# Kernel tuning notes

Hardware: AMD Instinct MI355X
Metric: run time of the kernel (lower is better)

## Reference

```python
import jax, jax.numpy as jnp
import numpy as np

H = W = 64          # input_resolution
C = 256             # dim
HEADS = 8
WS = 8              # window_size
SHIFT = WS // 2
DEPTH = 2           # block 0: no shift, block 1: shifted + mask
HIDDEN = 4 * C      # mlp_ratio * dim
B = 8
N = WS * WS                 # tokens per window
NW = (H // WS) * (W // WS)  # windows per image
EPS = 1e-5


def _rel_pos_index():
    coords = np.stack(np.meshgrid(np.arange(WS), np.arange(WS), indexing='ij')).reshape(2, -1)
    rel = (coords[:, :, None] - coords[:, None, :]).transpose(1, 2, 0)
    rel[:, :, 0] += WS - 1
    rel[:, :, 1] += WS - 1
    rel[:, :, 0] *= 2 * WS - 1
    return rel.sum(-1)  # [N, N] indices into (2*ws-1)^2 table

REL_IDX = jnp.asarray(_rel_pos_index())


def _attn_mask():
    # Swin shift mask: label 3x3 regions, compare window-token labels
    img = np.zeros((H, W))
    slices = (slice(0, -WS), slice(-WS, -SHIFT), slice(-SHIFT, None))
    cnt = 0
    for hs in slices:
        for ws_ in slices:
            img[hs, ws_] = cnt
            cnt += 1
    mw = img.reshape(H // WS, WS, W // WS, WS).transpose(0, 2, 1, 3).reshape(-1, N)
    diff = mw[:, None, :] - mw[:, :, None]
    return jnp.asarray(np.where(diff != 0, -100.0, 0.0), dtype=np.float32)  # [nW, N, N]

ATTN_MASK = _attn_mask()


def layernorm(x, g, b):
    mu = jnp.mean(x, axis=-1, keepdims=True)
    var = jnp.mean((x - mu) ** 2, axis=-1, keepdims=True)
    return (x - mu) * jax.lax.rsqrt(var + EPS) * g + b


def setup_inputs() -> dict:
    key = jax.random.key(0)
    ks = jax.random.split(key, 6)
    s = 0.02
    return {
        'x': jax.random.normal(ks[0], (B, H * W, C), jnp.float32),
        'qkv_w': jax.random.normal(ks[1], (DEPTH, C, 3 * C), jnp.float32) * s,
        'qkv_b': jnp.zeros((DEPTH, 3 * C), jnp.float32),
        'proj_w': jax.random.normal(ks[2], (DEPTH, C, C), jnp.float32) * s,
        'proj_b': jnp.zeros((DEPTH, C), jnp.float32),
        'ln1_g': jnp.ones((DEPTH, C), jnp.float32),
        'ln1_b': jnp.zeros((DEPTH, C), jnp.float32),
        'ln2_g': jnp.ones((DEPTH, C), jnp.float32),
        'ln2_b': jnp.zeros((DEPTH, C), jnp.float32),
        'fc1_w': jax.random.normal(ks[3], (DEPTH, C, HIDDEN), jnp.float32) * s,
        'fc1_b': jnp.zeros((DEPTH, HIDDEN), jnp.float32),
        'fc2_w': jax.random.normal(ks[4], (DEPTH, HIDDEN, C), jnp.float32) * s,
        'fc2_b': jnp.zeros((DEPTH, C), jnp.float32),
        'rpb': jax.random.normal(ks[5], (DEPTH, (2 * WS - 1) ** 2, HEADS), jnp.float32) * s,
    }


def window_attention(xw, qw, qb, pw, pb, rpb_i, mask):
    # xw: [B*nW, N, C]
    B_ = xw.shape[0]
    d = C // HEADS
    qkv = (xw @ qw + qb).reshape(B_, N, 3, HEADS, d).transpose(2, 0, 3, 1, 4)
    q, k, v = qkv[0] * (d ** -0.5), qkv[1], qkv[2]   # [B_, h, N, d]
    attn = jnp.einsum('bhnd,bhmd->bhnm', q, k)
    bias = rpb_i[REL_IDX.reshape(-1)].reshape(N, N, HEADS).transpose(2, 0, 1)
    attn = attn + bias[None]
    if mask is not None:
        attn = attn.reshape(-1, NW, HEADS, N, N) + mask[None, :, None]
        attn = attn.reshape(-1, HEADS, N, N)
    attn = jax.nn.softmax(attn, axis=-1)
    out = jnp.einsum('bhnm,bhmd->bhnd', attn, v).transpose(0, 2, 1, 3).reshape(B_, N, C)
    return out @ pw + pb


def reference(x, qkv_w, qkv_b, proj_w, proj_b, ln1_g, ln1_b, ln2_g, ln2_b,
              fc1_w, fc1_b, fc2_w, fc2_b, rpb):
    for i in range(DEPTH):
        shift = 0 if i % 2 == 0 else SHIFT
        mask = None if shift == 0 else ATTN_MASK
        shortcut = x
        h = layernorm(x, ln1_g[i], ln1_b[i]).reshape(-1, H, W, C)
        if shift:
            h = jnp.roll(h, (-shift, -shift), axis=(1, 2))
        # window partition -> [B*nW, N, C]
        hw = h.reshape(-1, H // WS, WS, W // WS, WS, C).transpose(0, 1, 3, 2, 4, 5).reshape(-1, N, C)
        aw = window_attention(hw, qkv_w[i], qkv_b[i], proj_w[i], proj_b[i], rpb[i], mask)
        # window reverse
        h = aw.reshape(-1, H // WS, W // WS, WS, WS, C).transpose(0, 1, 3, 2, 4, 5).reshape(-1, H, W, C)
        if shift:
            h = jnp.roll(h, (shift, shift), axis=(1, 2))
        x = shortcut + h.reshape(-1, H * W, C)
        m = layernorm(x, ln2_g[i], ln2_b[i])
        m = jax.nn.gelu(m @ fc1_w[i] + fc1_b[i], approximate=False) @ fc2_w[i] + fc2_b[i]
        x = x + m
    return x
```

## Files before the change

### kernel.cpp

```cpp
#include <hip/hip_runtime.h>
#include <hip/hip_bf16.h>


typedef __hip_bfloat16 bf16;
typedef unsigned short u16;
typedef unsigned int u32;
typedef short short8 __attribute__((ext_vector_type(8)));
typedef float floatx4 __attribute__((ext_vector_type(4)));

#define DEVI static __device__ __forceinline__
#define WAITCNT_VM(n) asm volatile("s_waitcnt vmcnt(" #n ")" ::: "memory")

DEVI float lo16(u32 u) { union { u32 i; float f; } x; x.i = u << 16; return x.f; }
DEVI float hi16(u32 u) { union { u32 i; float f; } x; x.i = u & 0xffff0000u; return x.f; }
DEVI float b2f(u16 u) { union { u32 i; float f; } x; x.i = ((u32)u) << 16; return x.f; }
DEVI u16 f2b(float f) {
  union { float f; u32 i; } x; x.f = f;
  u32 r = x.i + 0x7fffu + ((x.i >> 16) & 1u);
  return (u16)(r >> 16);
}
DEVI float in_elem(const void* p, size_t i, int m) {
  return m ? b2f(((const u16*)p)[i]) : ((const float*)p)[i];
}
DEVI int swlab(int g) { return (g < 56) ? 0 : (g < 60 ? 1 : 2); }

DEVI float gelu_cheap(float v) {
  const float u = v * v;
  const float t = v * __builtin_fmaf(0.1029436f, u, 2.3022090f);
  const float e = __builtin_amdgcn_exp2f(t);
  const float r = __builtin_amdgcn_rcpf(e + 1.0f);
  return __builtin_fmaf(-v, r, v);
}

DEVI void async16(const bf16* g, bf16* l) {
  __builtin_amdgcn_global_load_lds((const __attribute__((address_space(1))) u32*)g,
                                   (__attribute__((address_space(3))) u32*)l, 16, 0, 0);
}

__global__ void k_detect(const u32* __restrict__ ln1g, int* __restrict__ mode) {
  if (threadIdx.x == 0 && blockIdx.x == 0)
    *mode = (ln1g[0] == 0x3F803F80u) ? 1 : 0;
}

__global__ __launch_bounds__(256) void k_ingest_ln(const void* __restrict__ xin,
    float* __restrict__ xf, const void* __restrict__ gamw, const void* __restrict__ betw,
    bf16* __restrict__ outp, const int* __restrict__ mode)
{
  const int m = *mode;
  const int l = threadIdx.x & 63, w = threadIdx.x >> 6;
  const int row = blockIdx.x * 4 + w;
  const int t = row & 63, win = row >> 6;
  const int bb = win >> 6, wi = win & 63;
  const int gh = ((wi >> 3) << 3) + (t >> 3);
  const int gw = ((wi & 7) << 3) + (t & 7);
  const int srow = (bb << 12) + (gh << 6) + gw;
  const int cb = l << 2;
  float4 v;
  if (m) {
    const uint2 u = *(const uint2*)((const u16*)xin + (size_t)srow * 256 + cb);
    v = make_float4(lo16(u.x), hi16(u.x), lo16(u.y), hi16(u.y));
  } else {
    v = ((const float4*)((const float*)xin + (size_t)srow * 256))[l];
  }
  ((float4*)(xf + (size_t)srow * 256))[l] = v;
  float s = v.x + v.y + v.z + v.w;
#pragma unroll
  for (int off = 32; off > 0; off >>= 1) s += __shfl_xor(s, off, 64);
  const float mu = s * 0.00390625f;
  const float a = v.x - mu, b = v.y - mu, c = v.z - mu, d = v.w - mu;
  float q = a * a + b * b + c * c + d * d;
#pragma unroll
  for (int off = 32; off > 0; off >>= 1) q += __shfl_xor(q, off, 64);
  const float rs = rsqrtf(q * 0.00390625f + 1e-5f);
  const float o0 = a * rs * in_elem(gamw, cb + 0, m) + in_elem(betw, cb + 0, m);
  const float o1 = b * rs * in_elem(gamw, cb + 1, m) + in_elem(betw, cb + 1, m);
  const float o2 = c * rs * in_elem(gamw, cb + 2, m) + in_elem(betw, cb + 2, m);
  const float o3 = d * rs * in_elem(gamw, cb + 3, m) + in_elem(betw, cb + 3, m);
  const u32 p0 = (u32)f2b(o0) | ((u32)f2b(o1) << 16);
  const u32 p1 = (u32)f2b(o2) | ((u32)f2b(o3) << 16);
  *(uint2*)((u16*)outp + (size_t)row * 256 + cb) = make_uint2(p0, p1);
}

__global__ __launch_bounds__(256) void k_transpose(
    const void* __restrict__ src, bf16* __restrict__ dst,
    const int* __restrict__ mode, int estride, int dstride, int R, int Cn) {
  __shared__ float T[32][33];
  const int m = *mode;
  const int tx = threadIdx.x & 31, ty = threadIdx.x >> 5;
  const int bc = blockIdx.x << 5, br = blockIdx.y << 5;
  for (int d = 0; d < 2; ++d) {
    __syncthreads();
#pragma unroll
    for (int dy = 0; dy < 4; ++dy) {
      const int r = br + ty + dy * 8;
      T[ty + dy * 8][tx] = in_elem(src, (size_t)d * estride + (size_t)r * Cn + bc + tx, m);
    }
    __syncthreads();
#pragma unroll
    for (int dy = 0; dy < 4; ++dy) {
      const int c = bc + ty + dy * 8;
      ((u16*)dst)[(size_t)d * dstride + (size_t)c * R + br + tx] = f2b(T[tx][ty + dy * 8]);
    }
  }
}

template <int EPI>
__global__ __launch_bounds__(256, 3) void k_gemm(
    const bf16* __restrict__ A, const bf16* __restrict__ Bt,
    const void* __restrict__ bias, bf16* __restrict__ outb,
    const int* __restrict__ mode, int boff, int K, int N)
{
  __shared__ __align__(16) bf16 As[3][128 * 32];
  __shared__ __align__(16) bf16 Bs[3][128 * 32];
  __shared__ __align__(16) float EPs[4][4][72];
  const int md = *mode;
  const int tid = threadIdx.x;
  const int l = tid & 63, wid = tid >> 6;
  const int wr = wid >> 1, wc = wid & 1;

  const int gx = gridDim.x;
  const int nwg = gx * gridDim.y;
  int fid = blockIdx.y * gx + blockIdx.x;
  if (!(nwg & 7)) fid = (fid & 7) * (nwg >> 3) + (fid >> 3);
  const int row0 = (fid / gx) * 128;
  const int col0 = (fid % gx) * 128;

  const int lrow = l >> 2;
  const int lkof = (((l & 3) ^ ((l >> 3) & 3)) * 8);
  const int qsw  = (((l >> 4) ^ ((l >> 1) & 3)) * 8);

  floatx4 acc[4][4];
#pragma unroll
  for (int mi = 0; mi < 4; ++mi)
#pragma unroll
    for (int ni = 0; ni < 4; ++ni)
      acc[mi][ni] = (floatx4){0.f, 0.f, 0.f, 0.f};

  auto stage = [&](int b, int kbase) {
    const int kk = kbase + lkof;
#pragma unroll
    for (int c = 0; c < 2; ++c) {
      const int seg = c * 4 + wid;
      async16(A + (size_t)(row0 + seg * 16 + lrow) * K + kk, &As[b][seg * 512]);
      async16(Bt + (size_t)(col0 + seg * 16 + lrow) * K + kk, &Bs[b][seg * 512]);
    }
  };

  const int nsl = K >> 5;
  stage(0, 0);
  stage(1, 32);

  for (int s = 0; s < nsl; ++s) {
    const int cur = s % 3;
    if (s < nsl - 1) { WAITCNT_VM(4); }
    else            { WAITCNT_VM(0); }
    __builtin_amdgcn_s_barrier();
    if (s + 2 < nsl) stage((s + 2) % 3, (s + 2) * 32);

    short8 af[4], bq[4];
#pragma unroll
    for (int mi = 0; mi < 4; ++mi)
      af[mi] = *(const short8*)&As[cur][(wr * 64 + mi * 16 + (l & 15)) * 32 + qsw];
#pragma unroll
    for (int ni = 0; ni < 4; ++ni)
      bq[ni] = *(const short8*)&Bs[cur][(wc * 64 + ni * 16 + (l & 15)) * 32 + qsw];
#pragma unroll
    for (int mi = 0; mi < 4; ++mi)
#pragma unroll
      for (int ni = 0; ni < 4; ++ni)
        acc[mi][ni] = __builtin_amdgcn_mfma_f32_16x16x32_bf16(af[mi], bq[ni], acc[mi][ni], 0, 0, 0);
  }

  float* EPw = &EPs[wid][0][0];
  const int cl = l & 15, rq = l >> 4;
  const int colb = wc * 64 + cl * 4;
  float bias4[4];
#pragma unroll
  for (int i = 0; i < 4; ++i) bias4[i] = in_elem(bias, (size_t)boff + col0 + colb + i, md);

#pragma unroll
  for (int mi = 0; mi < 4; ++mi) {
#pragma unroll
    for (int r = 0; r < 4; ++r) {
#pragma unroll
      for (int ni = 0; ni < 4; ++ni)
        EPw[rq * 72 + ni * 16 + cl] = acc[mi][ni][r];
      const float4 av = *(const float4*)&EPw[rq * 72 + cl * 4];
      float v0 = av.x + bias4[0], v1 = av.y + bias4[1];
      float v2 = av.z + bias4[2], v3 = av.w + bias4[3];
      if (EPI == 1) {
        v0 = gelu_cheap(v0); v1 = gelu_cheap(v1);
        v2 = gelu_cheap(v2); v3 = gelu_cheap(v3);
      }
      const int row = row0 + wr * 64 + mi * 16 + rq * 4 + r;
      const u32 p0 = (u32)f2b(v0) | ((u32)f2b(v1) << 16);
      const u32 p1 = (u32)f2b(v2) | ((u32)f2b(v3) << 16);
      *(uint2*)((u16*)outb + (size_t)row * N + col0 + colb) = make_uint2(p0, p1);
    }
  }
}

template <int MODE>
__global__ __launch_bounds__(256, 2) void k_fullN(
    const bf16* __restrict__ A, const bf16* __restrict__ Bt,
    const void* __restrict__ bias, const void* __restrict__ lng,
    const void* __restrict__ lnb, void* __restrict__ outp,
    float* __restrict__ xf, const int* __restrict__ mode,
    int boff, int lnoff, int K, int shift)
{
  __shared__ __align__(16) char smem[61440];
  bf16* As = (bf16*)smem;
  bf16* Bs = (bf16*)(smem + 12288);
  const int md = *mode;
  const int tid = threadIdx.x;
  const int l = tid & 63, w = tid >> 6;

  int fid = blockIdx.x;
  const int nwg = gridDim.x;
  if (!(nwg & 7)) fid = (fid & 7) * (nwg >> 3) + (fid >> 3);
  const int row0 = fid * 64;

  const int lrow = l >> 2;
  const int lkof = (((l & 3) ^ ((l >> 3) & 3)) * 8);
  const int qsw  = (((l >> 4) ^ ((l >> 1) & 3)) * 8);

  floatx4 acc[16];
#pragma unroll
  for (int ni = 0; ni < 16; ++ni) acc[ni] = (floatx4){0.f, 0.f, 0.f, 0.f};

  auto stage = [&](int b, int kbase) {
    const int kk = kbase + lkof;
    async16(A + (size_t)(row0 + w * 16 + lrow) * K + kk, As + b * 2048 + w * 512);
#pragma unroll
    for (int c = 0; c < 4; ++c) {
      const int seg = c * 4 + w;
      async16(Bt + (size_t)(seg * 16 + lrow) * K + kk, Bs + b * 8192 + seg * 512);
    }
  };

  const int nsl = K >> 5;
  stage(0, 0);
  stage(1, 32);

  for (int s = 0; s < nsl; ++s) {
    const int cur = s % 3;
    if (s < nsl - 1) { WAITCNT_VM(5); }
    else            { WAITCNT_VM(0); }
    __builtin_amdgcn_s_barrier();
    if (s + 2 < nsl) stage((s + 2) % 3, (s + 2) * 32);

    const short8 af = *(const short8*)&As[cur * 2048 + (w * 16 + (l & 15)) * 32 + qsw];
#pragma unroll
    for (int ni = 0; ni < 16; ++ni) {
      const short8 bq = *(const short8*)&Bs[cur * 8192 + (ni * 16 + (l & 15)) * 32 + qsw];
      acc[ni] = __builtin_amdgcn_mfma_f32_16x16x32_bf16(af, bq, acc[ni], 0, 0, 0);
    }
  }

  __syncthreads();

  float* EPw = (float*)smem + w * 1088;
  const int cl = l & 15, rq = l >> 4;
  const int c4 = l * 4;

  float bias4[4], g4[4], b4[4];
#pragma unroll
  for (int i = 0; i < 4; ++i) bias4[i] = in_elem(bias, (size_t)boff + c4 + i, md);
  if (MODE != 2) {
#pragma unroll
    for (int i = 0; i < 4; ++i) {
      g4[i] = in_elem(lng, (size_t)lnoff + c4 + i, md);
      b4[i] = in_elem(lnb, (size_t)lnoff + c4 + i, md);
    }
  }

  for (int r = 0; r < 4; ++r) {
#pragma unroll
    for (int ni = 0; ni < 16; ++ni)
      EPw[rq * 272 + ni * 16 + cl] = acc[ni][r];

#pragma unroll
    for (int g = 0; g < 4; ++g) {
      const int lrow_g = row0 + w * 16 + g * 4 + r;
      const float4 av = *(const float4*)&EPw[g * 272 + c4];

      int resrow, dstrow;
      if (MODE == 0) {
        const int t_ = lrow_g & 63, win = lrow_g >> 6;
        const int bb = win >> 6, wi2 = win & 63;
        int gh = ((wi2 >> 3) << 3) + (t_ >> 3);
        int gw = ((wi2 & 7) << 3) + (t_ & 7);
        gh = (gh + shift) & 63; gw = (gw + shift) & 63;
        resrow = (bb << 12) + (gh << 6) + gw;
        dstrow = resrow;
      } else if (MODE == 1) {
        resrow = lrow_g;
        const int bb = lrow_g >> 12, th = (lrow_g >> 6) & 63, tw = lrow_g & 63;
        const int gh = (th + 60) & 63, gw = (tw + 60) & 63;
        const int wi2 = ((gh >> 3) << 3) + (gw >> 3);
        const int tt = ((gh & 7) << 3) + (gw & 7);
        dstrow = (bb << 12) + (wi2 << 6) + tt;
      } else {
        resrow = lrow_g; dstrow = lrow_g;
      }

      const float4 xv = *(const float4*)(xf + (size_t)resrow * 256 + c4);
      float t0 = av.x + bias4[0] + xv.x;
      float t1 = av.y + bias4[1] + xv.y;
      float t2 = av.z + bias4[2] + xv.z;
      float t3 = av.w + bias4[3] + xv.w;

      if (MODE == 2) {
        *(float4*)((float*)outp + (size_t)lrow_g * 256 + c4) = make_float4(t0, t1, t2, t3);
        continue;
      }

      float s = t0 + t1 + t2 + t3;
#pragma unroll
      for (int off = 32; off > 0; off >>= 1) s += __shfl_xor(s, off, 64);
      const float mu = s * 0.00390625f;
      const float d0 = t0 - mu, d1 = t1 - mu, d2 = t2 - mu, d3 = t3 - mu;
      float q = d0 * d0 + d1 * d1 + d2 * d2 + d3 * d3;
#pragma unroll
      for (int off = 32; off > 0; off >>= 1) q += __shfl_xor(q, off, 64);
      const float rs = rsqrtf(q * 0.00390625f + 1e-5f);

      *(float4*)(xf + (size_t)resrow * 256 + c4) = make_float4(t0, t1, t2, t3);
      const u32 p0 = (u32)f2b(d0 * rs * g4[0] + b4[0]) | ((u32)f2b(d1 * rs * g4[1] + b4[1]) << 16);
      const u32 p1 = (u32)f2b(d2 * rs * g4[2] + b4[2]) | ((u32)f2b(d3 * rs * g4[3] + b4[3]) << 16);
      *(uint2*)((u16*)outp + (size_t)dstrow * 256 + c4) = make_uint2(p0, p1);
    }
  }
}

__global__ __launch_bounds__(256, 2) void k_attn(
    const bf16* __restrict__ qkv, const void* __restrict__ rpb,
    bf16* __restrict__ outp, const int* __restrict__ mode, int eoff, int shifted)
{
  __shared__ __align__(16) u16 Pl[4][64][72];
  __shared__ __align__(16) u16 Vt[4][32][72];
  __shared__ float rpbs[4][228];
  const int md = *mode;
  const int l = threadIdx.x & 63, w = threadIdx.x >> 6;
  const int cl = l & 15, qd = l >> 4;
  const int ko = qd * 8;
  const int win = blockIdx.x;
  const int wi = win & 63;
  const int whb = (wi >> 3) << 3, wwb = (wi & 7) << 3;
  const size_t rowbase = (size_t)win * 64 * 768;

  for (int hh = 0; hh < 2; ++hh) {
    const int h = w + hh * 4;
    for (int i = l; i < 225; i += 64)
      rpbs[w][i] = in_elem(rpb, (size_t)eoff + (size_t)i * 8 + h, md);
    {
      const u16* vrow = (const u16*)(qkv + rowbase + (size_t)l * 768 + 512 + h * 32);
#pragma unroll
      for (int n = 0; n < 32; ++n) Vt[w][n][l] = vrow[n];
    }
    short8 qf[4], kf[4];
#pragma unroll
    for (int t = 0; t < 4; ++t) {
      qf[t] = *(const short8*)(qkv + rowbase + (size_t)(t * 16 + cl) * 768 + h * 32 + ko);
      kf[t] = *(const short8*)(qkv + rowbase + (size_t)(t * 16 + cl) * 768 + 256 + h * 32 + ko);
    }
    __syncthreads();

    floatx4 S[4][4];
#pragma unroll
    for (int mi = 0; mi < 4; ++mi)
#pragma unroll
      for (int ni = 0; ni < 4; ++ni)
        S[mi][ni] = __builtin_amdgcn_mfma_f32_16x16x32_bf16(qf[mi], kf[ni], (floatx4){0.f, 0.f, 0.f, 0.f}, 0, 0, 0);

    int cty[4], ctx[4], clab[4];
#pragma unroll
    for (int ni = 0; ni < 4; ++ni) {
      const int ct = ni * 16 + cl;
      cty[ni] = ct >> 3; ctx[ni] = ct & 7;
      clab[ni] = shifted ? (swlab(whb + cty[ni]) * 3 + swlab(wwb + ctx[ni])) : 0;
    }

    float invs[4][4];
#pragma unroll
    for (int mi = 0; mi < 4; ++mi) {
#pragma unroll
      for (int r = 0; r < 4; ++r) {
        const int rt = mi * 16 + qd * 4 + r;
        const int rty = rt >> 3, rtx = rt & 7;
        const int rlab = shifted ? (swlab(whb + rty) * 3 + swlab(wwb + rtx)) : 0;
        float sv[4];
#pragma unroll
        for (int ni = 0; ni < 4; ++ni) {
          float x = S[mi][ni][r] * 0.17677669529663687f;
          x += rpbs[w][(rty - cty[ni] + 7) * 15 + (rtx - ctx[ni] + 7)];
          if (shifted && (rlab != clab[ni])) x -= 100.f;
          sv[ni] = x;
        }
        float mx = fmaxf(fmaxf(sv[0], sv[1]), fmaxf(sv[2], sv[3]));
        mx = fmaxf(mx, __shfl_xor(mx, 1, 64));
        mx = fmaxf(mx, __shfl_xor(mx, 2, 64));
        mx = fmaxf(mx, __shfl_xor(mx, 4, 64));
        mx = fmaxf(mx, __shfl_xor(mx, 8, 64));
        float sum = 0.f;
#pragma unroll
        for (int ni = 0; ni < 4; ++ni) { sv[ni] = __expf(sv[ni] - mx); sum += sv[ni]; }
        sum += __shfl_xor(sum, 1, 64);
        sum += __shfl_xor(sum, 2, 64);
        sum += __shfl_xor(sum, 4, 64);
        sum += __shfl_xor(sum, 8, 64);
        invs[mi][r] = __builtin_amdgcn_rcpf(sum);
#pragma unroll
        for (int ni = 0; ni < 4; ++ni) Pl[w][rt][ni * 16 + cl] = f2b(sv[ni]);
      }
    }
    __syncthreads();

    floatx4 O[4][2];
#pragma unroll
    for (int mi = 0; mi < 4; ++mi)
#pragma unroll
      for (int nv = 0; nv < 2; ++nv)
        O[mi][nv] = (floatx4){0.f, 0.f, 0.f, 0.f};
    short8 vf[2][2];
#pragma unroll
    for (int nv = 0; nv < 2; ++nv)
#pragma unroll
      for (int kk = 0; kk < 2; ++kk)
        vf[nv][kk] = *(const short8*)&Vt[w][nv * 16 + cl][kk * 32 + ko];
#pragma unroll
    for (int mi = 0; mi < 4; ++mi) {
      const short8 pf0 = *(const short8*)&Pl[w][mi * 16 + cl][ko];
      const short8 pf1 = *(const short8*)&Pl[w][mi * 16 + cl][32 + ko];
#pragma unroll
      for (int nv = 0; nv < 2; ++nv) {
        O[mi][nv] = __builtin_amdgcn_mfma_f32_16x16x32_bf16(pf0, vf[nv][0], O[mi][nv], 0, 0, 0);
        O[mi][nv] = __builtin_amdgcn_mfma_f32_16x16x32_bf16(pf1, vf[nv][1], O[mi][nv], 0, 0, 0);
      }
    }

#pragma unroll
    for (int mi = 0; mi < 4; ++mi)
#pragma unroll
      for (int nv = 0; nv < 2; ++nv)
#pragma unroll
        for (int r = 0; r < 4; ++r) {
          const int row = mi * 16 + qd * 4 + r;
          ((u16*)outp)[((size_t)win * 64 + row) * 256 + h * 32 + nv * 16 + cl] =
              f2b(O[mi][nv][r] * invs[mi][r]);
        }
    __syncthreads();
  }
}

extern "C" void kernel_launch(void* const* d_in, const int* in_sizes, int n_in,
                              void* d_out, int out_size, void* d_ws, size_t ws_size,
                              hipStream_t stream) {
  (void)in_sizes; (void)n_in; (void)out_size; (void)ws_size;
  const void* x_in   = d_in[0];
  const void* qkv_w  = d_in[1];
  const void* qkv_b  = d_in[2];
  const void* proj_w = d_in[3];
  const void* proj_b = d_in[4];
  const void* ln1_g  = d_in[5];
  const void* ln1_b  = d_in[6];
  const void* ln2_g  = d_in[7];
  const void* ln2_b  = d_in[8];
  const void* fc1_w  = d_in[9];
  const void* fc1_b  = d_in[10];
  const void* fc2_w  = d_in[11];
  const void* fc2_b  = d_in[12];
  const void* rpb    = d_in[13];

  char* ws = (char*)d_ws;
  float* xf  = (float*)ws;
  bf16* bufH = (bf16*)(ws + 33554432);
  bf16* bufQ = (bf16*)(ws + 100663296);
  bf16* bufB = (bf16*)(ws + 150994944);
  bf16* wT   = (bf16*)(ws + 167772160);
  int* mode  = (int*)(ws + 170917888);

  k_detect<<<1, 1, 0, stream>>>((const u32*)ln1_g, mode);
  k_ingest_ln<<<8192, 256, 0, stream>>>(x_in, xf, ln1_g, ln1_b, bufB, mode);

  k_transpose<<<dim3(24, 8), 256, 0, stream>>>(qkv_w,  wT,          mode, 196608, 786432, 256, 768);
  k_transpose<<<dim3(8, 8), 256, 0, stream>>>(proj_w, wT + 196608, mode, 65536, 786432, 256, 256);
  k_transpose<<<dim3(32, 8), 256, 0, stream>>>(fc1_w, wT + 262144, mode, 262144, 786432, 256, 1024);
  k_transpose<<<dim3(8, 32), 256, 0, stream>>>(fc2_w, wT + 524288, mode, 262144, 786432, 1024, 256);

  for (int i = 0; i < 2; ++i) {
    const int shift = i ? 4 : 0;
    bf16* base  = wT + (size_t)i * 786432;
    bf16* qkvT  = base;
    bf16* projT = base + 196608;
    bf16* fc1T  = base + 262144;
    bf16* fc2T  = base + 524288;

    k_gemm<0><<<dim3(6, 256), 256, 0, stream>>>(bufB, qkvT, qkv_b, bufQ, mode, i * 768, 256, 768);
    k_attn<<<512, 256, 0, stream>>>(bufQ, rpb, bufB, mode, i * 1800, i);
    k_fullN<0><<<512, 256, 0, stream>>>(bufB, projT, proj_b, ln2_g, ln2_b, bufB, xf, mode,
                                        i * 256, i * 256, 256, shift);
    k_gemm<1><<<dim3(8, 256), 256, 0, stream>>>(bufB, fc1T, fc1_b, bufH, mode, i * 1024, 256, 1024);
    if (i == 0)
      k_fullN<1><<<512, 256, 0, stream>>>(bufH, fc2T, fc2_b, ln1_g, ln1_b, bufB, xf, mode,
                                          0, 256, 1024, 4);
    else
      k_fullN<2><<<512, 256, 0, stream>>>(bufH, fc2T, fc2_b, nullptr, nullptr, d_out, xf, mode,
                                          256, 0, 1024, 0);
  }
}
```

Before: 424.8 us.

## Fuse fc1, GELU and fc2 into one MLP kernel keeping hidden in LDS

Adds a k_mlp kernel that computes fc1 per 128-column hidden chunk, applies GELU, stores the chunk as bf16 in shared memory, and immediately accumulates it into the fc2 output. It then runs the residual add and LayerNorm (or the final output write) in the same epilogue. This removes the 8192x1024 bf16 hidden buffer round trip through global memory and one kernel launch per block. k_fullN is reduced to the projection path only. In exchange each block now uses 80 KB of LDS, which may reduce occupancy, and the whole fc1+fc2 chain is serialized within one 64-row tile across 512 blocks.

After: 421.2 us. About the same (-0.8%).

```diff
diff --git a/kernel.cpp b/kernel.cpp
--- a/kernel.cpp
+++ b/kernel.cpp
@@ -266,12 +266,10 @@
   float bias4[4], g4[4], b4[4];
 #pragma unroll
   for (int i = 0; i < 4; ++i) bias4[i] = in_elem(bias, (size_t)boff + c4 + i, md);
-  if (MODE != 2) {
-#pragma unroll
-    for (int i = 0; i < 4; ++i) {
-      g4[i] = in_elem(lng, (size_t)lnoff + c4 + i, md);
-      b4[i] = in_elem(lnb, (size_t)lnoff + c4 + i, md);
-    }
+#pragma unroll
+  for (int i = 0; i < 4; ++i) {
+    g4[i] = in_elem(lng, (size_t)lnoff + c4 + i, md);
+    b4[i] = in_elem(lnb, (size_t)lnoff + c4 + i, md);
   }
 
   for (int r = 0; r < 4; ++r) {
@@ -284,25 +282,13 @@
       const int lrow_g = row0 + w * 16 + g * 4 + r;
       const float4 av = *(const float4*)&EPw[g * 272 + c4];
 
-      int resrow, dstrow;
-      if (MODE == 0) {
-        const int t_ = lrow_g & 63, win = lrow_g >> 6;
-        const int bb = win >> 6, wi2 = win & 63;
-        int gh = ((wi2 >> 3) << 3) + (t_ >> 3);
-        int gw = ((wi2 & 7) << 3) + (t_ & 7);
-        gh = (gh + shift) & 63; gw = (gw + shift) & 63;
-        resrow = (bb << 12) + (gh << 6) + gw;
-        dstrow = resrow;
-      } else if (MODE == 1) {
-        resrow = lrow_g;
-        const int bb = lrow_g >> 12, th = (lrow_g >> 6) & 63, tw = lrow_g & 63;
-        const int gh = (th + 60) & 63, gw = (tw + 60) & 63;
-        const int wi2 = ((gh >> 3) << 3) + (gw >> 3);
-        const int tt = ((gh & 7) << 3) + (gw & 7);
-        dstrow = (bb << 12) + (wi2 << 6) + tt;
-      } else {
-        resrow = lrow_g; dstrow = lrow_g;
-      }
+      const int t_ = lrow_g & 63, win = lrow_g >> 6;
+      const int bb = win >> 6, wi2 = win & 63;
+      int gh = ((wi2 >> 3) << 3) + (t_ >> 3);
+      int gw = ((wi2 & 7) << 3) + (t_ & 7);
+      gh = (gh + shift) & 63; gw = (gw + shift) & 63;
+      const int resrow = (bb << 12) + (gh << 6) + gw;
+      const int dstrow = resrow;
 
       const float4 xv = *(const float4*)(xf + (size_t)resrow * 256 + c4);
       float t0 = av.x + bias4[0] + xv.x;
@@ -310,11 +296,6 @@
       float t2 = av.z + bias4[2] + xv.z;
       float t3 = av.w + bias4[3] + xv.w;
 
-      if (MODE == 2) {
-        *(float4*)((float*)outp + (size_t)lrow_g * 256 + c4) = make_float4(t0, t1, t2, t3);
-        continue;
-      }
-
       float s = t0 + t1 + t2 + t3;
 #pragma unroll
       for (int off = 32; off > 0; off >>= 1) s += __shfl_xor(s, off, 64);
@@ -326,6 +307,170 @@
       const float rs = rsqrtf(q * 0.00390625f + 1e-5f);
 
       *(float4*)(xf + (size_t)resrow * 256 + c4) = make_float4(t0, t1, t2, t3);
+      const u32 p0 = (u32)f2b(d0 * rs * g4[0] + b4[0]) | ((u32)f2b(d1 * rs * g4[1] + b4[1]) << 16);
+      const u32 p1 = (u32)f2b(d2 * rs * g4[2] + b4[2]) | ((u32)f2b(d3 * rs * g4[3] + b4[3]) << 16);
+      *(uint2*)((u16*)outp + (size_t)dstrow * 256 + c4) = make_uint2(p0, p1);
+    }
+  }
+}
+
+template <int MODE>
+__global__ __launch_bounds__(256) void k_mlp(
+    const bf16* __restrict__ A, const bf16* __restrict__ W1t, const bf16* __restrict__ W2t,
+    const void* __restrict__ b1, const void* __restrict__ b2,
+    const void* __restrict__ lng, const void* __restrict__ lnb,
+    void* __restrict__ outp, float* __restrict__ xf, const int* __restrict__ mode,
+    int b1off, int b2off, int lnoff)
+{
+  __shared__ __align__(16) char smem[81920];
+  bf16* Al = (bf16*)smem;
+  bf16* Wl = (bf16*)(smem + 32768);
+  u16*  Hl = (u16*)(smem + 65536);
+  const int md = *mode;
+  const int tid = threadIdx.x;
+  const int l = tid & 63, w = tid >> 6;
+  int fid = blockIdx.x;
+  const int nwg = gridDim.x;
+  if (!(nwg & 7)) fid = (fid & 7) * (nwg >> 3) + (fid >> 3);
+  const int row0 = fid * 64;
+
+  const int lr4 = l >> 2;
+  const int lkof = (((l & 3) ^ ((l >> 3) & 3)) * 8);
+  const int qsw  = (((l >> 4) ^ ((l >> 1) & 3)) * 8);
+  const int cl = l & 15, rq = l >> 4;
+
+  floatx4 acc2[16];
+#pragma unroll
+  for (int ni = 0; ni < 16; ++ni) acc2[ni] = (floatx4){0.f, 0.f, 0.f, 0.f};
+
+  auto stageW1 = [&](int c, int s, int b) {
+#pragma unroll
+    for (int cc = 0; cc < 2; ++cc) {
+      const int seg = w * 2 + cc;
+      const size_t gr = (size_t)(c * 128 + seg * 16 + lr4) * 256;
+      async16(W1t + gr + s * 32 + lkof,       Wl + b * 8192 + seg * 512);
+      async16(W1t + gr + (s + 1) * 32 + lkof, Wl + b * 8192 + 4096 + seg * 512);
+    }
+  };
+  auto stageW2 = [&](int c, int q, int b) {
+#pragma unroll
+    for (int cc = 0; cc < 4; ++cc) {
+      const int seg = w * 4 + cc;
+      async16(W2t + (size_t)(seg * 16 + lr4) * 1024 + c * 128 + q * 32 + lkof,
+              Wl + b * 8192 + seg * 512);
+    }
+  };
+
+#pragma unroll
+  for (int s = 0; s < 8; ++s)
+    async16(A + (size_t)(row0 + w * 16 + lr4) * 256 + s * 32 + lkof, Al + s * 2048 + w * 512);
+  stageW1(0, 0, 0);
+
+  int buf = 0;
+  for (int c = 0; c < 8; ++c) {
+    floatx4 acc1[8];
+#pragma unroll
+    for (int ni = 0; ni < 8; ++ni) acc1[ni] = (floatx4){0.f, 0.f, 0.f, 0.f};
+
+    for (int p = 0; p < 4; ++p) {
+      __syncthreads();
+      if (p < 3) stageW1(c, 2 * (p + 1), buf ^ 1);
+      else       stageW2(c, 0, buf ^ 1);
+      const short8 af0 = *(const short8*)&Al[(2 * p) * 2048 + (w * 16 + cl) * 32 + qsw];
+      const short8 af1 = *(const short8*)&Al[(2 * p + 1) * 2048 + (w * 16 + cl) * 32 + qsw];
+#pragma unroll
+      for (int ni = 0; ni < 8; ++ni) {
+        const short8 bq0 = *(const short8*)(Wl + buf * 8192 + (ni * 16 + cl) * 32 + qsw);
+        acc1[ni] = __builtin_amdgcn_mfma_f32_16x16x32_bf16(af0, bq0, acc1[ni], 0, 0, 0);
+      }
+#pragma unroll
+      for (int ni = 0; ni < 8; ++ni) {
+        const short8 bq1 = *(const short8*)(Wl + buf * 8192 + 4096 + (ni * 16 + cl) * 32 + qsw);
+        acc1[ni] = __builtin_amdgcn_mfma_f32_16x16x32_bf16(af1, bq1, acc1[ni], 0, 0, 0);
+      }
+      buf ^= 1;
+    }
+
+#pragma unroll
+    for (int ni = 0; ni < 8; ++ni) {
+      const int hc = ni * 16 + cl;
+      const float bv = in_elem(b1, (size_t)b1off + c * 128 + hc, md);
+      const int hbase = (hc >> 5) * 2048;
+      const int hq = (hc >> 3) & 3, he = hc & 7;
+#pragma unroll
+      for (int r = 0; r < 4; ++r) {
+        const int hr = w * 16 + rq * 4 + r;
+        Hl[hbase + hr * 32 + ((hq ^ ((hr >> 1) & 3)) * 8) + he] =
+            f2b(gelu_cheap(acc1[ni][r] + bv));
+      }
+    }
+
+    for (int q = 0; q < 4; ++q) {
+      __syncthreads();
+      if (q < 3)      stageW2(c, q + 1, buf ^ 1);
+      else if (c < 7) stageW1(c + 1, 0, buf ^ 1);
+      const short8 hf = *(const short8*)((const bf16*)&Hl[q * 2048 + (w * 16 + cl) * 32 + qsw]);
+#pragma unroll
+      for (int ni = 0; ni < 16; ++ni) {
+        const short8 bq = *(const short8*)(Wl + buf * 8192 + (ni * 16 + cl) * 32 + qsw);
+        acc2[ni] = __builtin_amdgcn_mfma_f32_16x16x32_bf16(hf, bq, acc2[ni], 0, 0, 0);
+      }
+      buf ^= 1;
+    }
+  }
+
+  __syncthreads();
+  float* EPw = (float*)smem + w * 1088;
+  const int c4 = l * 4;
+
+  float bias4[4], g4[4], b4[4];
+#pragma unroll
+  for (int i = 0; i < 4; ++i) bias4[i] = in_elem(b2, (size_t)b2off + c4 + i, md);
+  if (MODE == 1) {
+#pragma unroll
+    for (int i = 0; i < 4; ++i) {
+      g4[i] = in_elem(lng, (size_t)lnoff + c4 + i, md);
+      b4[i] = in_elem(lnb, (size_t)lnoff + c4 + i, md);
+    }
+  }
+
+  for (int r = 0; r < 4; ++r) {
+#pragma unroll
+    for (int ni = 0; ni < 16; ++ni)
+      EPw[rq * 272 + ni * 16 + cl] = acc2[ni][r];
+
+#pragma unroll
+    for (int g = 0; g < 4; ++g) {
+      const int lrow_g = row0 + w * 16 + g * 4 + r;
+      const float4 av = *(const float4*)&EPw[g * 272 + c4];
+      const float4 xv = *(const float4*)(xf + (size_t)lrow_g * 256 + c4);
+      float t0 = av.x + bias4[0] + xv.x;
+      float t1 = av.y + bias4[1] + xv.y;
+      float t2 = av.z + bias4[2] + xv.z;
+      float t3 = av.w + bias4[3] + xv.w;
+
+      if (MODE == 2) {
+        *(float4*)((float*)outp + (size_t)lrow_g * 256 + c4) = make_float4(t0, t1, t2, t3);
+        continue;
+      }
+
+      const int bb = lrow_g >> 12, th = (lrow_g >> 6) & 63, tw = lrow_g & 63;
+      const int gh = (th + 60) & 63, gw = (tw + 60) & 63;
+      const int wi2 = ((gh >> 3) << 3) + (gw >> 3);
+      const int tt = ((gh & 7) << 3) + (gw & 7);
+      const int dstrow = (bb << 12) + (wi2 << 6) + tt;
+
+      float s = t0 + t1 + t2 + t3;
+#pragma unroll
+      for (int off = 32; off > 0; off >>= 1) s += __shfl_xor(s, off, 64);
+      const float mu = s * 0.00390625f;
+      const float d0 = t0 - mu, d1 = t1 - mu, d2 = t2 - mu, d3 = t3 - mu;
+      float q = d0 * d0 + d1 * d1 + d2 * d2 + d3 * d3;
+#pragma unroll
+      for (int off = 32; off > 0; off >>= 1) q += __shfl_xor(q, off, 64);
+      const float rs = rsqrtf(q * 0.00390625f + 1e-5f);
+
+      *(float4*)(xf + (size_t)lrow_g * 256 + c4) = make_float4(t0, t1, t2, t3);
       const u32 p0 = (u32)f2b(d0 * rs * g4[0] + b4[0]) | ((u32)f2b(d1 * rs * g4[1] + b4[1]) << 16);
       const u32 p1 = (u32)f2b(d2 * rs * g4[2] + b4[2]) | ((u32)f2b(d3 * rs * g4[3] + b4[3]) << 16);
       *(uint2*)((u16*)outp + (size_t)dstrow * 256 + c4) = make_uint2(p0, p1);
@@ -474,7 +619,6 @@
 
   char* ws = (char*)d_ws;
   float* xf  = (float*)ws;
-  bf16* bufH = (bf16*)(ws + 33554432);
   bf16* bufQ = (bf16*)(ws + 100663296);
   bf16* bufB = (bf16*)(ws + 150994944);
   bf16* wT   = (bf16*)(ws + 167772160);
@@ -498,14 +642,13 @@
 
     k_gemm<0><<<dim3(6, 256), 256, 0, stream>>>(bufB, qkvT, qkv_b, bufQ, mode, i * 768, 256, 768);
     k_attn<<<512, 256, 0, stream>>>(bufQ, rpb, bufB, mode, i * 1800, i);
-    k_fullN<0><<<512, 256, 0, stream>>>(bufB, projT, proj_b, ln2_g, ln2_b, bufB, xf, mode,
+    k_fullN<0><<<512, 256, 0, stream>>>(bufB, projT, proj_b, ln2_g, ln2_b, bufQ, xf, mode,
                                         i * 256, i * 256, 256, shift);
-    k_gemm<1><<<dim3(8, 256), 256, 0, stream>>>(bufB, fc1T, fc1_b, bufH, mode, i * 1024, 256, 1024);
     if (i == 0)
-      k_fullN<1><<<512, 256, 0, stream>>>(bufH, fc2T, fc2_b, ln1_g, ln1_b, bufB, xf, mode,
-                                          0, 256, 1024, 4);
+      k_mlp<1><<<512, 256, 0, stream>>>(bufQ, fc1T, fc2T, fc1_b, fc2_b, ln1_g, ln1_b,
+                                        bufB, xf, mode, 0, 0, 256);
     else
-      k_fullN<2><<<512, 256, 0, stream>>>(bufH, fc2T, fc2_b, nullptr, nullptr, d_out, xf, mode,
-                                          256, 0, 1024, 0);
-  }
-}
+      k_mlp<2><<<512, 256, 0, stream>>>(bufQ, fc1T, fc2T, fc1_b, fc2_b, nullptr, nullptr,
+                                        d_out, xf, mode, 1024, 256, 0);
+  }
+}
```
